# Performance work log

Measured on AMD Instinct MI355X. Metric: run time of the kernel, lower is better.

Reference implementation:

```python
import jax, jax.numpy as jnp
import numpy as np

B, T, S, D = 8, 2048, 8, 256


def setup_inputs() -> dict:
    key = jax.random.key(0)
    k1, k2, k3 = jax.random.split(key, 3)
    x = jax.random.normal(k1, (B, T, S, D), dtype=jnp.float32)
    # nn.Linear-style init scale ~ 1/sqrt(fan_in)
    W_in = jax.random.normal(k2, (D, 2 * D), dtype=jnp.float32) / np.sqrt(D)
    b_in = jnp.zeros((2 * D,), dtype=jnp.float32)
    W_out = jax.random.normal(k3, (D, D), dtype=jnp.float32) / np.sqrt(D)
    b_out = jnp.zeros((D,), dtype=jnp.float32)
    return {"x": x, "W_in": W_in, "b_in": b_in, "W_out": W_out, "b_out": b_out}


def reference(x, W_in, b_in, W_out, b_out):
    # in_proj then chunk into gate / candidate (matches torch chunk(2, dim=-1))
    h = jnp.einsum("btsd,de->btse", x, W_in) + b_in  # [B,T,S,2D]
    gate, cand = jnp.split(h, 2, axis=-1)
    alpha = jax.nn.sigmoid(gate)
    cand = jnp.tanh(cand)
    # Diagonal linear recurrence: state_t = a_t * state_{t-1} + b_t
    # with a_t = 1 - alpha_t, b_t = alpha_t * cand_t, state_{-1} = 0.
    a = 1.0 - alpha
    b = alpha * cand

    def combine(c1, c2):
        a1, b1 = c1
        a2, b2 = c2
        return a1 * a2, a2 * b1 + b2

    _, y = jax.lax.associative_scan(combine, (a, b), axis=1)  # [B,T,S,D]
    # dropout is identity in eval mode
    return jnp.einsum("btsd,de->btse", y, W_out) + b_out
```

## Files before the change

kernel.cpp:

```cpp
#include <hip/hip_runtime.h>
#include <hip/hip_bf16.h>
#include <hip/hip_fp16.h>
#include <cstdint>

typedef __attribute__((ext_vector_type(4))) float f32x4;
typedef __attribute__((ext_vector_type(8))) short s16x8;

#define DEVI static __device__ __forceinline__

constexpr int Bc = 8, Tc = 2048, Sc = 8, Dc = 256;
constexpr int Mc = Bc * Tc * Sc;

DEVI unsigned short f2bf(float x) {
  return __bfloat16_as_ushort(__float2bfloat16(x));
}

DEVI f32x4 mfma16(s16x8 a, s16x8 b, f32x4 c) {
  return __builtin_amdgcn_mfma_f32_16x16x32_bf16(a, b, c, 0, 0, 0);
}

DEVI void gld16(const void* g, void* l) {
  __builtin_amdgcn_global_load_lds(
      (const __attribute__((address_space(1))) unsigned int*)g,
      (__attribute__((address_space(3))) unsigned int*)l, 16, 0, 0);
}

__global__ void cvt_x_k(const float* __restrict__ in, unsigned short* __restrict__ out, int n) {
  int i = (blockIdx.x * blockDim.x + threadIdx.x) * 8;
  int stride = gridDim.x * blockDim.x * 8;
  for (; i < n; i += stride) {
    f32x4 a = *(const f32x4*)(in + i);
    f32x4 b = *(const f32x4*)(in + i + 4);
    s16x8 o;
    o[0] = (short)f2bf(a[0]); o[1] = (short)f2bf(a[1]);
    o[2] = (short)f2bf(a[2]); o[3] = (short)f2bf(a[3]);
    o[4] = (short)f2bf(b[0]); o[5] = (short)f2bf(b[1]);
    o[6] = (short)f2bf(b[2]); o[7] = (short)f2bf(b[3]);
    *(s16x8*)(out + i) = o;
  }
}

__global__ void cvtW_k(const float* __restrict__ Win, const float* __restrict__ Wout,
                       unsigned short* __restrict__ wtin, unsigned short* __restrict__ wtout) {
  int tid = blockIdx.x * blockDim.x + threadIdx.x;
  if (tid < 512 * 256) {
    int c = tid >> 8, r = tid & 255;
    wtin[tid] = f2bf(Win[r * 512 + c]);
  } else {
    int t = tid - 512 * 256;
    int c = t >> 8, r = t & 255;
    wtout[t] = f2bf(Wout[r * 256 + c]);
  }
}

__global__ __launch_bounds__(512, 2) void g1scan_k(
    const unsigned short* __restrict__ xb,
    const unsigned short* __restrict__ wt,
    const float* __restrict__ bias,
    unsigned short* __restrict__ yb)
{
  __shared__ unsigned short As[2][8 * 64 * 32];
  __shared__ unsigned int   abuf[64 * 32];
  __shared__ float segA[16][32], segB[16][32];

  int bid = blockIdx.x;
  int lb = (bid & 7) * 64 + (bid >> 3);
  int b = lb >> 6, s = (lb >> 3) & 7, dq = lb & 7;
  int tid = threadIdx.x;
  int lane = tid & 63, wave = tid >> 6;
  int rg = wave >> 1, cg = wave & 1;

  const short* xs = (const short*)xb;
  const short* wsrc = (const short*)wt;
  size_t rowbase = (size_t)b * 16384 + s;

  int cl = cg * 16 + (lane & 15);
  int kg = (lane >> 4) * 8;

  s16x8 bGr[8], bCr[8];
  #pragma unroll
  for (int kf = 0; kf < 8; ++kf) {
    bGr[kf] = *(const s16x8*)(wsrc + (size_t)(dq * 32 + cl) * 256 + kf * 32 + kg);
    bCr[kf] = *(const s16x8*)(wsrc + (size_t)(256 + dq * 32 + cl) * 256 + kf * 32 + kg);
  }
  float bg = bias[dq * 32 + cl];
  float bc = bias[256 + dq * 32 + cl];

  const short* pA[4];
  int ldso[4];
  #pragma unroll
  for (int q = 0; q < 4; ++q) {
    int j = q * 512 + tid;
    int kf = j >> 8, rem = j & 255, r = rem >> 2, cc = rem & 3;
    pA[q] = xs + (rowbase + (size_t)r * 8) * 256 + kf * 32 + cc * 8;
    ldso[q] = j * 8;
  }
  const size_t ASTRIDE = (size_t)64 * 8 * 256;

  #pragma unroll
  for (int q = 0; q < 4; ++q) gld16(pA[q], (unsigned short*)As[0] + ldso[q]);
  #pragma unroll
  for (int q = 0; q < 4; ++q) gld16(pA[q] + ASTRIDE, (unsigned short*)As[1] + ldso[q]);
  #pragma unroll
  for (int q = 0; q < 4; ++q) pA[q] += 2 * ASTRIDE;

  float stt = 0.f;

  __syncthreads();

  for (int ch = 0; ch < 32; ++ch) {
    int cur = ch & 1;
    const unsigned short* Ab = (const unsigned short*)As[cur];

    f32x4 accG = {}, accC = {};
    #pragma unroll
    for (int kf = 0; kf < 8; ++kf) {
      s16x8 aF = *(const s16x8*)(Ab + kf * 2048 + (rg * 16 + (lane & 15)) * 32 + kg);
      accG = mfma16(aF, bGr[kf], accG);
      accC = mfma16(aF, bCr[kf], accC);
    }

    unsigned pk[4];
    #pragma unroll
    for (int r = 0; r < 4; ++r) {
      float g = accG[r] + bg;
      float c = accC[r] + bc;
      float alpha = 1.f / (1.f + __expf(-g));
      float e2 = __expf(2.f * c);
      float th = 1.f - 2.f / (e2 + 1.f);
      __half2 h;
      h.x = __float2half(1.f - alpha);
      h.y = __float2half(alpha * th);
      pk[r] = *(unsigned*)&h;
    }
    #pragma unroll
    for (int r = 0; r < 4; ++r) {
      int trow = rg * 16 + (lane >> 4) * 4 + r;
      abuf[trow * 32 + cl] = pk[r];
    }

    __syncthreads();

    int sid = wave * 2 + (lane >> 5), dd = lane & 31;
    float av[4], bv[4];
    float A = 1.f, Bv = 0.f;
    #pragma unroll
    for (int u = 0; u < 4; ++u) {
      unsigned vv = abuf[(sid * 4 + u) * 32 + dd];
      __half2 h = *(__half2*)&vv;
      av[u] = __half2float(h.x);
      bv[u] = __half2float(h.y);
      A = av[u] * A;
      Bv = fmaf(av[u], Bv, bv[u]);
    }
    segA[sid][dd] = A;
    segB[sid][dd] = Bv;

    __syncthreads();

    if (ch + 2 < 32) {
      #pragma unroll
      for (int q = 0; q < 4; ++q) gld16(pA[q], (unsigned short*)As[cur] + ldso[q]);
      #pragma unroll
      for (int q = 0; q < 4; ++q) pA[q] += ASTRIDE;
    }

    float sin = stt, s_w = stt;
    #pragma unroll
    for (int w2 = 0; w2 < 16; ++w2) {
      if (w2 == sid) s_w = sin;
      sin = fmaf(segA[w2][dd], sin, segB[w2][dd]);
    }
    stt = sin;

    size_t ybase = (rowbase + (size_t)(ch * 64 + sid * 4) * 8) * 256 + dq * 32 + dd;
    float sv = s_w;
    #pragma unroll
    for (int u = 0; u < 4; ++u) {
      sv = fmaf(av[u], sv, bv[u]);
      yb[ybase + (size_t)u * 8 * 256] = f2bf(sv);
    }
  }
}

__global__ __launch_bounds__(256, 2) void gemm2_k(
    const unsigned short* __restrict__ yb,
    const unsigned short* __restrict__ wt,
    const float* __restrict__ bias,
    float* __restrict__ out)
{
  __shared__ unsigned short As[2][2][128 * 32];
  __shared__ unsigned short Bs[2][2][128 * 32];

  int bid = blockIdx.x;
  int swz = (bid & 7) * 256 + (bid >> 3);
  int mtile = swz >> 1, ctile = swz & 1;
  int tid = threadIdx.x;
  int lane = tid & 63, wave = tid >> 6;
  int wr = wave >> 1, wc = wave & 1;

  const short* ys = (const short*)yb;
  const short* wsrc = (const short*)wt;

  auto STAGE = [&](int buf, int k0) {
    unsigned short* Ad = &As[buf][0][0];
    unsigned short* Bd = &Bs[buf][0][0];
    #pragma unroll
    for (int q = 0; q < 4; ++q) {
      int j = q * 256 + tid;
      int p = j >> 9, r = (j >> 2) & 127, cc = j & 3;
      int koff = k0 + p * 32 + cc * 8;
      gld16(ys + (size_t)(mtile * 128 + r) * 256 + koff, Ad + (size_t)j * 8);
      gld16(wsrc + (size_t)(ctile * 128 + r) * 256 + koff, Bd + (size_t)j * 8);
    }
  };

  f32x4 acc[4][4] = {};

  STAGE(0, 0);
  __syncthreads();
  #pragma unroll
  for (int kk = 0; kk < 4; ++kk) {
    int cur = kk & 1;
    if (kk < 3) STAGE(cur ^ 1, (kk + 1) * 64);
    int kg = (lane >> 4) * 8;
    #pragma unroll
    for (int ks = 0; ks < 2; ++ks) {
      s16x8 aF[4], bF[4];
      #pragma unroll
      for (int mf = 0; mf < 4; ++mf)
        aF[mf] = *(const s16x8*)&As[cur][ks][(wr * 64 + mf * 16 + (lane & 15)) * 32 + kg];
      #pragma unroll
      for (int nf = 0; nf < 4; ++nf)
        bF[nf] = *(const s16x8*)&Bs[cur][ks][(wc * 64 + nf * 16 + (lane & 15)) * 32 + kg];
      #pragma unroll
      for (int mf = 0; mf < 4; ++mf)
        #pragma unroll
        for (int nf = 0; nf < 4; ++nf)
          acc[mf][nf] = mfma16(aF[mf], bF[nf], acc[mf][nf]);
    }
    if (kk < 3) __syncthreads();
  }

  int orow0 = mtile * 128 + wr * 64 + (lane >> 4) * 4;
  #pragma unroll
  for (int nf = 0; nf < 4; ++nf) {
    int col = ctile * 128 + wc * 64 + nf * 16 + (lane & 15);
    float bo = bias[col];
    #pragma unroll
    for (int mf = 0; mf < 4; ++mf) {
      #pragma unroll
      for (int r = 0; r < 4; ++r) {
        int row = orow0 + mf * 16 + r;
        out[(size_t)row * 256 + col] = acc[mf][nf][r] + bo;
      }
    }
  }
}

extern "C" void kernel_launch(void* const* d_in, const int* in_sizes, int n_in,
                              void* d_out, int out_size, void* d_ws, size_t ws_size,
                              hipStream_t stream)
{
  const float* x    = (const float*)d_in[0];
  const float* Win  = (const float*)d_in[1];
  const float* bin  = (const float*)d_in[2];
  const float* Wout = (const float*)d_in[3];
  const float* bout = (const float*)d_in[4];
  float* out = (float*)d_out;
  char* ws = (char*)d_ws;

  unsigned short* wtin  = (unsigned short*)(ws);
  unsigned short* wtout = (unsigned short*)(ws + 262144);
  unsigned short* yb    = (unsigned short*)(ws + 393216);
  unsigned short* xb    = (unsigned short*)(ws + 393216 + (size_t)Mc * 256 * 2);

  cvt_x_k<<<1024, 256, 0, stream>>>(x, xb, Mc * 256);
  cvtW_k<<<768, 256, 0, stream>>>(Win, Wout, wtin, wtout);
  g1scan_k<<<512, 512, 0, stream>>>(xb, wtin, bin, yb);
  gemm2_k<<<2048, 256, 0, stream>>>(yb, wtout, bout, out);
}
```

Measured before the change: 181.6 us.

## Replace LDS transpose scan with in-register wave shuffle scan

New measurement: 172.5 us. 1.05x faster.

```diff
diff --git a/kernel.cpp b/kernel.cpp
--- a/kernel.cpp
+++ b/kernel.cpp
@@ -60,8 +60,7 @@
     unsigned short* __restrict__ yb)
 {
   __shared__ unsigned short As[2][8 * 64 * 32];
-  __shared__ unsigned int   abuf[64 * 32];
-  __shared__ float segA[16][32], segB[16][32];
+  __shared__ float segA[2][4][32], segB[2][4][32];
 
   int bid = blockIdx.x;
   int lb = (bid & 7) * 64 + (bid >> 3);
@@ -69,13 +68,14 @@
   int tid = threadIdx.x;
   int lane = tid & 63, wave = tid >> 6;
   int rg = wave >> 1, cg = wave & 1;
+  int lo = lane & 15, hi = lane >> 4;
 
   const short* xs = (const short*)xb;
   const short* wsrc = (const short*)wt;
   size_t rowbase = (size_t)b * 16384 + s;
 
-  int cl = cg * 16 + (lane & 15);
-  int kg = (lane >> 4) * 8;
+  int cl = cg * 16 + lo;
+  int kg = hi * 8;
 
   s16x8 bGr[8], bCr[8];
   #pragma unroll
@@ -91,7 +91,7 @@
   #pragma unroll
   for (int q = 0; q < 4; ++q) {
     int j = q * 512 + tid;
-    int kf = j >> 8, rem = j & 255, r = rem >> 2, cc = rem & 3;
+    int kf = j >> 8, rem = j & 255, r = rem >> 2, cc = j & 3;
     pA[q] = xs + (rowbase + (size_t)r * 8) * 256 + kf * 32 + cc * 8;
     ldso[q] = j * 8;
   }
@@ -115,12 +115,12 @@
     f32x4 accG = {}, accC = {};
     #pragma unroll
     for (int kf = 0; kf < 8; ++kf) {
-      s16x8 aF = *(const s16x8*)(Ab + kf * 2048 + (rg * 16 + (lane & 15)) * 32 + kg);
+      s16x8 aF = *(const s16x8*)(Ab + kf * 2048 + (rg * 16 + lo) * 32 + kg);
       accG = mfma16(aF, bGr[kf], accG);
       accC = mfma16(aF, bCr[kf], accC);
     }
 
-    unsigned pk[4];
+    float av[4], bv[4];
     #pragma unroll
     for (int r = 0; r < 4; ++r) {
       float g = accG[r] + bg;
@@ -128,36 +128,28 @@
       float alpha = 1.f / (1.f + __expf(-g));
       float e2 = __expf(2.f * c);
       float th = 1.f - 2.f / (e2 + 1.f);
-      __half2 h;
-      h.x = __float2half(1.f - alpha);
-      h.y = __float2half(alpha * th);
-      pk[r] = *(unsigned*)&h;
-    }
-    #pragma unroll
-    for (int r = 0; r < 4; ++r) {
-      int trow = rg * 16 + (lane >> 4) * 4 + r;
-      abuf[trow * 32 + cl] = pk[r];
-    }
+      av[r] = 1.f - alpha;
+      bv[r] = alpha * th;
+    }
+
+    float iA = av[0], iB = bv[0];
+    #pragma unroll
+    for (int r = 1; r < 4; ++r) { iA = iA * av[r]; iB = fmaf(av[r], iB, bv[r]); }
+
+    {
+      float tA = __shfl_up(iA, 16), tB = __shfl_up(iB, 16);
+      float nA = tA * iA, nB = fmaf(iA, tB, iB);
+      if (hi >= 1) { iA = nA; iB = nB; }
+      tA = __shfl_up(iA, 32); tB = __shfl_up(iB, 32);
+      nA = tA * iA; nB = fmaf(iA, tB, iB);
+      if (hi >= 2) { iA = nA; iB = nB; }
+    }
+    float eA = __shfl_up(iA, 16), eB = __shfl_up(iB, 16);
+    if (hi == 0) { eA = 1.f; eB = 0.f; }
+    if (hi == 3) { segA[cur][rg][cl] = iA; segB[cur][rg][cl] = iB; }
 
     __syncthreads();
 
-    int sid = wave * 2 + (lane >> 5), dd = lane & 31;
-    float av[4], bv[4];
-    float A = 1.f, Bv = 0.f;
-    #pragma unroll
-    for (int u = 0; u < 4; ++u) {
-      unsigned vv = abuf[(sid * 4 + u) * 32 + dd];
-      __half2 h = *(__half2*)&vv;
-      av[u] = __half2float(h.x);
-      bv[u] = __half2float(h.y);
-      A = av[u] * A;
-      Bv = fmaf(av[u], Bv, bv[u]);
-    }
-    segA[sid][dd] = A;
-    segB[sid][dd] = Bv;
-
-    __syncthreads();
-
     if (ch + 2 < 32) {
       #pragma unroll
       for (int q = 0; q < 4; ++q) gld16(pA[q], (unsigned short*)As[cur] + ldso[q]);
@@ -165,16 +157,16 @@
       for (int q = 0; q < 4; ++q) pA[q] += ASTRIDE;
     }
 
-    float sin = stt, s_w = stt;
-    #pragma unroll
-    for (int w2 = 0; w2 < 16; ++w2) {
-      if (w2 == sid) s_w = sin;
-      sin = fmaf(segA[w2][dd], sin, segB[w2][dd]);
-    }
-    stt = sin;
-
-    size_t ybase = (rowbase + (size_t)(ch * 64 + sid * 4) * 8) * 256 + dq * 32 + dd;
-    float sv = s_w;
+    float run = stt, s_w = stt;
+    #pragma unroll
+    for (int r2 = 0; r2 < 4; ++r2) {
+      if (r2 == rg) s_w = run;
+      run = fmaf(segA[cur][r2][cl], run, segB[cur][r2][cl]);
+    }
+    stt = run;
+
+    float sv = fmaf(eA, s_w, eB);
+    size_t ybase = (rowbase + (size_t)(ch * 64 + rg * 16 + hi * 4) * 8) * 256 + dq * 32 + cl;
     #pragma unroll
     for (int u = 0; u < 4; ++u) {
       sv = fmaf(av[u], sv, bv[u]);
```
